# Performance work log

Hardware: AMD Instinct MI355X
Metric: run time of the kernel (lower is better)

The kernel has to match this reference:

```python
import jax, jax.numpy as jnp
import numpy as np

C_IN, C_OUT, ORDER, BATCH, N = 4, 8, 3, 8, 512
STDV = 1.0 / 3.0


def setup_inputs() -> dict:
    key = jax.random.key(0)
    k0, k1, k2, k3, k4 = jax.random.split(key, 5)
    s_in = jax.random.normal(k0, (C_IN, BATCH, N, N), dtype=jnp.float32)
    a_o = jax.random.normal(k1, (BATCH, N, N), dtype=jnp.float32)
    alpha = jax.random.normal(k2, (C_OUT, C_IN), dtype=jnp.float32) * STDV + 1.0
    beta = jax.random.normal(k3, (C_OUT, C_IN), dtype=jnp.float32) * STDV + 0.0
    coeffs = jax.random.normal(k4, (C_OUT, ORDER + 1, C_IN), dtype=jnp.float32) * STDV
    coeffs = coeffs.at[:, 1, :].set(1.0)  # torch init sets linear Cheb coeff to 1
    tau = jnp.linspace(0.01, 0.9, C_OUT).astype(jnp.float32).reshape(C_OUT, 1, 1, 1)
    return {"s_in": s_in, "a_o": a_o, "alpha": alpha, "beta": beta,
            "coeffs": coeffs, "tau": tau}


def _cheb_terms(A, n_terms):
    # Chebyshev matrix polynomial basis: T0=I, T1=A, T_k = 2*A@T_{k-1} - T_{k-2}
    b, n, _ = A.shape
    terms = [jnp.broadcast_to(jnp.eye(n, dtype=A.dtype), (b, n, n)), A]
    for _ in range(2, n_terms):
        terms.append(2.0 * jnp.matmul(A, terms[-1]) - terms[-2])
    return jnp.stack(terms[:n_terms])  # (n_terms, b, n, n)


def reference(s_in, a_o, alpha, beta, coeffs, tau):
    # s_in: (c_in, B, N, N); a_o: (B, N, N)
    c_out, n_terms, c_in = coeffs.shape
    n = a_o.shape[-1]
    # mimo_tensor_polynomial with cob='cheb': a_o is identical across c_in,
    # so compute the Cheb basis once on (B,N,N) and contract with coeffs.
    T = _cheb_terms(a_o, n_terms)                      # (K+1, B, N, N)
    poly = jnp.einsum('oki,kbnm->oibnm', coeffs, T)    # (c_out, c_in, B, N, N)
    # a@a_o + a_o@a is independent of c_out (broadcast in torch), compute once
    mix = jnp.matmul(s_in, a_o) + jnp.matmul(a_o, s_in)  # (c_in, B, N, N)
    temp = (alpha[:, :, None, None, None] * s_in
            + beta[:, :, None, None, None] * mix
            + poly)                                     # (c_out, c_in, B, N, N)
    zd = 1.0 - jnp.eye(n, dtype=temp.dtype)             # zero diagonal mask
    temp = temp * zd
    temp = jnp.mean(temp, axis=1)                       # (c_out, B, N, N)
    # normalize_slices(which_norm='max_abs'): per (c_out, batch) slice
    mx = jnp.max(jnp.abs(temp), axis=(-2, -1), keepdims=True)
    temp = temp / jnp.where(mx == 0, jnp.ones_like(mx), mx)
    return jax.nn.relu(temp - tau)
```

## Files before the change

### kernel.cpp

```cpp
#include <hip/hip_runtime.h>

#define NDIM 512
#define NN (512*512)

typedef float          fv4  __attribute__((ext_vector_type(4)));
typedef unsigned int   uv2  __attribute__((ext_vector_type(2)));
typedef unsigned int   uv4  __attribute__((ext_vector_type(4)));
typedef unsigned short usv4 __attribute__((ext_vector_type(4)));
typedef unsigned short usv8 __attribute__((ext_vector_type(8)));
typedef short          sv8  __attribute__((ext_vector_type(8)));

__device__ __forceinline__ unsigned short f2bf(float x){
    unsigned u = __builtin_bit_cast(unsigned, x);
    u += 0x7fffu + ((u >> 16) & 1u);
    return (unsigned short)(u >> 16);
}
__device__ __forceinline__ float bf2f(unsigned short s){
    unsigned u = ((unsigned)s) << 16;
    return __builtin_bit_cast(float, u);
}

#define MFMA16(acc, va, vb) \
    acc = __builtin_amdgcn_mfma_f32_16x16x32_bf16( \
        __builtin_bit_cast(sv8, va), __builtin_bit_cast(sv8, vb), acc, 0, 0, 0)

#define TRREAD(dst, addr) \
    asm volatile("ds_read_b64_tr_b16 %0, %1" : "=v"(dst) : "v"(addr))

__global__ __launch_bounds__(256) void preconv_kernel(
    const float* __restrict__ s_in, const float* __restrict__ a_o,
    unsigned short* __restrict__ s_bf, unsigned short* __restrict__ Ah,
    unsigned short* __restrict__ Al)
{
    const int z  = blockIdx.y;
    const int e0 = blockIdx.x * 1024 + threadIdx.x * 4;
    if (z < 32) {
        float4 v = *(const float4*)(s_in + z * NN + e0);
        float vv[4] = {v.x, v.y, v.z, v.w};
        usv4 o;
        #pragma unroll
        for (int j = 0; j < 4; ++j) o[j] = f2bf(vv[j]);
        *(usv4*)(s_bf + z * NN + e0) = o;
    } else {
        const int b = z - 32;
        float4 v = *(const float4*)(a_o + b * NN + e0);
        float vv[4] = {v.x, v.y, v.z, v.w};
        usv4 h, l;
        #pragma unroll
        for (int j = 0; j < 4; ++j) {
            unsigned short hb = f2bf(vv[j]);
            h[j] = hb;
            l[j] = f2bf(vv[j] - bf2f(hb));
        }
        *(usv4*)(Ah + b * NN + e0) = h;
        *(usv4*)(Al + b * NN + e0) = l;
    }
}

__device__ __forceinline__ void stage_x8(const unsigned short* __restrict__ X,
                                         int row0, int k0, int tid,
                                         unsigned short (*__restrict__ H)[40]){
    #pragma unroll
    for (int it = 0; it < 2; ++it) {
        int f = tid + it * 256;
        int r = f >> 2, c8 = (f & 3) << 3;
        *(usv8*)&H[r][c8] = *(const usv8*)(X + (row0 + r) * NDIM + k0 + c8);
    }
}
__device__ __forceinline__ void stage_b8(const unsigned short* __restrict__ Y,
                                         int col0, int k0, int tid,
                                         unsigned short* __restrict__ Bs){
    #pragma unroll
    for (int it = 0; it < 2; ++it) {
        int f  = tid + it * 256;
        int kl = f & 3, h = (f >> 2) & 1, cs = (f >> 3) & 7, kh = f >> 6;
        int k  = kh * 4 + kl;
        *(usv8*)&Bs[cs * 512 + k * 16 + h * 8] =
            *(const usv8*)(Y + (k0 + k) * NDIM + col0 + cs * 16 + h * 8);
    }
}

__global__ __launch_bounds__(256) void gemm_fused_kernel(
    const unsigned short* __restrict__ s_bf,
    const unsigned short* __restrict__ Ah, const unsigned short* __restrict__ Al,
    unsigned short* __restrict__ AAh, unsigned short* __restrict__ AAl,
    float* __restrict__ AA, float* __restrict__ AAA,
    unsigned short* __restrict__ MIXbf, int stage)
{
    const int z = blockIdx.z;
    const bool split = (stage == 0) || (z < 8);

    const unsigned short *X1, *X2, *Y1, *Y2;
    if (stage == 0)      { X1 = Ah + z * NN;  X2 = Al + z * NN;
                           Y1 = Ah + z * NN;  Y2 = Al + z * NN; }
    else if (z < 8)      { X1 = Ah + z * NN;  X2 = Al + z * NN;
                           Y1 = AAh + z * NN; Y2 = AAl + z * NN; }
    else                 { const int z2 = z - 8, b = z2 & 7;
                           X1 = s_bf + z2 * NN; X2 = Ah + b * NN;
                           Y1 = Ah + b * NN;    Y2 = s_bf + z2 * NN; }

    const int row0 = blockIdx.y * 128, col0 = blockIdx.x * 128;
    const int tid = threadIdx.x, lane = tid & 63, w = tid >> 6;

    __shared__ unsigned short Xa[128][40], Xb[128][40];
    __shared__ unsigned short Ba[4096], Bb[4096];

    fv4 acc[4][4];
    #pragma unroll
    for (int mi = 0; mi < 4; ++mi)
        #pragma unroll
        for (int ni = 0; ni < 4; ++ni) acc[mi][ni] = (fv4)0.f;

    const unsigned ba_base = (unsigned)(uintptr_t)&Ba[0];
    const unsigned bb_base = (unsigned)(uintptr_t)&Bb[0];
    const unsigned laneoff = (((unsigned)lane >> 4) << 7) | (((unsigned)lane & 15) << 3);
    const unsigned wcol    = ((unsigned)(w & 1)) << 12;

    for (int k0 = 0; k0 < NDIM; k0 += 32) {
        stage_x8(X1, row0, k0, tid, Xa);
        stage_x8(X2, row0, k0, tid, Xb);
        stage_b8(Y1, col0, k0, tid, Ba);
        stage_b8(Y2, col0, k0, tid, Bb);
        __syncthreads();

        uv2 fa[4][2], fb[4][2];
        #pragma unroll
        for (int ni = 0; ni < 4; ++ni)
            #pragma unroll
            for (int h = 0; h < 2; ++h) {
                TRREAD(fa[ni][h], ba_base + wcol + laneoff + ni * 1024 + h * 512);
                TRREAD(fb[ni][h], bb_base + wcol + laneoff + ni * 1024 + h * 512);
            }
        asm volatile("s_waitcnt lgkmcnt(0)" ::: "memory");
        __builtin_amdgcn_sched_barrier(0);

        const int g4 = (lane >> 4) * 4;
        #pragma unroll
        for (int mi = 0; mi < 4; ++mi) {
            const unsigned short* xr1 = &Xa[(w >> 1) * 64 + mi * 16 + (lane & 15)][0];
            const unsigned short* xr2 = &Xb[(w >> 1) * 64 + mi * 16 + (lane & 15)][0];
            uv2 a0 = *(const uv2*)(xr1 + g4);
            uv2 a1 = *(const uv2*)(xr1 + 16 + g4);
            uv2 b0 = *(const uv2*)(xr2 + g4);
            uv2 b1 = *(const uv2*)(xr2 + 16 + g4);
            uv4 xa = {a0.x, a0.y, a1.x, a1.y};
            uv4 xb = {b0.x, b0.y, b1.x, b1.y};
            #pragma unroll
            for (int ni = 0; ni < 4; ++ni) {
                uv4 vba = {fa[ni][0].x, fa[ni][0].y, fa[ni][1].x, fa[ni][1].y};
                uv4 vbb = {fb[ni][0].x, fb[ni][0].y, fb[ni][1].x, fb[ni][1].y};
                if (split) {
                    MFMA16(acc[mi][ni], xa, vba);
                    MFMA16(acc[mi][ni], xa, vbb);
                    MFMA16(acc[mi][ni], xb, vba);
                } else {
                    MFMA16(acc[mi][ni], xa, vba);
                    MFMA16(acc[mi][ni], xb, vbb);
                }
            }
        }
        __syncthreads();
    }

    const int g = lane >> 4, c15 = lane & 15;
    if (split) {
        float* C = (stage == 0) ? (AA + z * NN) : (AAA + z * NN);
        #pragma unroll
        for (int mi = 0; mi < 4; ++mi)
            #pragma unroll
            for (int ni = 0; ni < 4; ++ni) {
                int r = row0 + (w >> 1) * 64 + mi * 16 + g * 4;
                int c = col0 + (w & 1) * 64 + ni * 16 + c15;
                #pragma unroll
                for (int q = 0; q < 4; ++q) {
                    float v = acc[mi][ni][q];
                    C[(r + q) * NDIM + c] = v;
                    if (stage == 0) {
                        unsigned short hb = f2bf(v);
                        AAh[z * NN + (r + q) * NDIM + c] = hb;
                        AAl[z * NN + (r + q) * NDIM + c] = f2bf(v - bf2f(hb));
                    }
                }
            }
    } else {
        unsigned short* Cm = MIXbf + (z - 8) * NN;
        #pragma unroll
        for (int mi = 0; mi < 4; ++mi)
            #pragma unroll
            for (int ni = 0; ni < 4; ++ni) {
                int r = row0 + (w >> 1) * 64 + mi * 16 + g * 4;
                int c = col0 + (w & 1) * 64 + ni * 16 + c15;
                #pragma unroll
                for (int q = 0; q < 4; ++q)
                    Cm[(r + q) * NDIM + c] = f2bf(acc[mi][ni][q]);
            }
    }
}

__global__ __launch_bounds__(256) void combine_kernel(
    const unsigned short* __restrict__ s_bf, const unsigned short* __restrict__ Ah,
    const float* __restrict__ AA, const float* __restrict__ AAA,
    const unsigned short* __restrict__ MIXbf,
    const float* __restrict__ alpha, const float* __restrict__ beta,
    const float* __restrict__ coeffs,
    float* __restrict__ out, unsigned short* __restrict__ tmp,
    unsigned int* __restrict__ smax, int use_tmp)
{
    const int b  = blockIdx.y;
    const int e0 = blockIdx.x * 2048 + threadIdx.x * 8;
    const int n  = e0 >> 9;
    const int m0 = e0 & 511;

    float ca[8], cb[8], cc[8];
    #pragma unroll
    for (int o = 0; o < 8; ++o) {
        float c1 = 0.f, c2 = 0.f, c3 = 0.f;
        #pragma unroll
        for (int i = 0; i < 4; ++i) {
            c1 += coeffs[o * 16 + 4 + i];
            c2 += coeffs[o * 16 + 8 + i];
            c3 += coeffs[o * 16 + 12 + i];
        }
        ca[o] = c1 - 3.f * c3; cb[o] = 2.f * c2; cc[o] = 4.f * c3;
    }

    float av[8], aav[8], aaav[8], sv[4][8], mv[4][8];
    {
        usv8 a8 = *(const usv8*)(Ah + b * NN + e0);
        #pragma unroll
        for (int j = 0; j < 8; ++j) av[j] = bf2f(a8[j]);
        const float4 q0 = *(const float4*)(AA + b * NN + e0);
        const float4 q1 = *(const float4*)(AA + b * NN + e0 + 4);
        aav[0]=q0.x; aav[1]=q0.y; aav[2]=q0.z; aav[3]=q0.w;
        aav[4]=q1.x; aav[5]=q1.y; aav[6]=q1.z; aav[7]=q1.w;
        const float4 r0 = *(const float4*)(AAA + b * NN + e0);
        const float4 r1 = *(const float4*)(AAA + b * NN + e0 + 4);
        aaav[0]=r0.x; aaav[1]=r0.y; aaav[2]=r0.z; aaav[3]=r0.w;
        aaav[4]=r1.x; aaav[5]=r1.y; aaav[6]=r1.z; aaav[7]=r1.w;
        #pragma unroll
        for (int i = 0; i < 4; ++i) {
            usv8 s8 = *(const usv8*)(s_bf + (i * 8 + b) * NN + e0);
            usv8 m8 = *(const usv8*)(MIXbf + (i * 8 + b) * NN + e0);
            #pragma unroll
            for (int j = 0; j < 8; ++j) { sv[i][j] = bf2f(s8[j]); mv[i][j] = bf2f(m8[j]); }
        }
    }

    float lmax[8];
    #pragma unroll
    for (int o = 0; o < 8; ++o) {
        float outv[8];
        float lm = 0.f;
        #pragma unroll
        for (int j = 0; j < 8; ++j) {
            float t = ca[o] * av[j] + cb[o] * aav[j] + cc[o] * aaav[j];
            #pragma unroll
            for (int i = 0; i < 4; ++i)
                t += alpha[o * 4 + i] * sv[i][j] + beta[o * 4 + i] * mv[i][j];
            t *= 0.25f;
            if (n == m0 + j) t = 0.f;
            outv[j] = t;
            lm = fmaxf(lm, fabsf(t));
        }
        lmax[o] = lm;
        if (use_tmp) {
            usv8 ov;
            #pragma unroll
            for (int j = 0; j < 8; ++j) ov[j] = f2bf(outv[j]);
            *(usv8*)(tmp + (o * 8 + b) * NN + e0) = ov;
        } else {
            *(float4*)(out + (o * 8 + b) * NN + e0) =
                make_float4(outv[0], outv[1], outv[2], outv[3]);
            *(float4*)(out + (o * 8 + b) * NN + e0 + 4) =
                make_float4(outv[4], outv[5], outv[6], outv[7]);
        }
    }

    #pragma unroll
    for (int o = 0; o < 8; ++o) {
        #pragma unroll
        for (int off = 32; off > 0; off >>= 1)
            lmax[o] = fmaxf(lmax[o], __shfl_xor(lmax[o], off, 64));
    }
    __shared__ float red[4][8];
    const int lane = threadIdx.x & 63, wv = threadIdx.x >> 6;
    if (lane == 0) {
        #pragma unroll
        for (int o = 0; o < 8; ++o) red[wv][o] = lmax[o];
    }
    __syncthreads();
    if (threadIdx.x < 8) {
        const int o = threadIdx.x;
        const float mfin = fmaxf(fmaxf(red[0][o], red[1][o]), fmaxf(red[2][o], red[3][o]));
        atomicMax(&smax[o * 8 + b], __float_as_uint(mfin));
    }
}

__global__ __launch_bounds__(256) void norm_kernel(
    float* __restrict__ out, const unsigned short* __restrict__ tmp,
    const unsigned int* __restrict__ smax, const float* __restrict__ tau,
    int use_tmp)
{
    const int ob = blockIdx.y;
    const float mx = __uint_as_float(smax[ob]);
    const float inv = (mx == 0.f) ? 1.f : (1.f / mx);
    const float t = tau[ob >> 3];
    const int e0 = blockIdx.x * 2048 + threadIdx.x * 8;
    float v[8];
    if (use_tmp) {
        usv8 tv = *(const usv8*)(tmp + ob * NN + e0);
        #pragma unroll
        for (int j = 0; j < 8; ++j) v[j] = bf2f(tv[j]);
    } else {
        float4 v0 = *(float4*)(out + ob * NN + e0);
        float4 v1 = *(float4*)(out + ob * NN + e0 + 4);
        v[0]=v0.x; v[1]=v0.y; v[2]=v0.z; v[3]=v0.w;
        v[4]=v1.x; v[5]=v1.y; v[6]=v1.z; v[7]=v1.w;
    }
    #pragma unroll
    for (int j = 0; j < 8; ++j) v[j] = fmaxf(fmaf(v[j], inv, -t), 0.f);
    *(float4*)(out + ob * NN + e0)     = make_float4(v[0], v[1], v[2], v[3]);
    *(float4*)(out + ob * NN + e0 + 4) = make_float4(v[4], v[5], v[6], v[7]);
}

extern "C" void kernel_launch(void* const* d_in, const int* in_sizes, int n_in,
                              void* d_out, int out_size, void* d_ws, size_t ws_size,
                              hipStream_t stream) {
    (void)in_sizes; (void)n_in; (void)out_size;
    const float* s_in   = (const float*)d_in[0];
    const float* a_o    = (const float*)d_in[1];
    const float* alpha  = (const float*)d_in[2];
    const float* beta   = (const float*)d_in[3];
    const float* coeffs = (const float*)d_in[4];
    const float* tau    = (const float*)d_in[5];
    float* out = (float*)d_out;

    float* AA  = (float*)d_ws;
    float* AAA = AA + 8 * NN;
    unsigned short* s_bf  = (unsigned short*)(AAA + 8 * NN);
    unsigned short* Ah    = s_bf + 32 * NN;
    unsigned short* Al    = Ah + 8 * NN;
    unsigned short* AAh   = Al + 8 * NN;
    unsigned short* AAl   = AAh + 8 * NN;
    unsigned short* MIXbf = AAl + 8 * NN;
    unsigned int* SMAX = (unsigned int*)(MIXbf + 32 * NN);
    unsigned short* TMP = (unsigned short*)(SMAX + 64);

    const size_t need_tmp = (size_t)((char*)(TMP + 64 * NN) - (char*)d_ws);
    const int use_tmp = (ws_size >= need_tmp) ? 1 : 0;

    hipLaunchKernelGGL(preconv_kernel, dim3(256, 40), dim3(256), 0, stream,
                       s_in, a_o, s_bf, Ah, Al);
    hipLaunchKernelGGL(gemm_fused_kernel, dim3(4, 4, 8), dim3(256), 0, stream,
                       s_bf, Ah, Al, AAh, AAl, AA, AAA, MIXbf, 0);
    hipLaunchKernelGGL(gemm_fused_kernel, dim3(4, 4, 40), dim3(256), 0, stream,
                       s_bf, Ah, Al, AAh, AAl, AA, AAA, MIXbf, 1);
    hipMemsetAsync(SMAX, 0, 64 * sizeof(unsigned int), stream);
    hipLaunchKernelGGL(combine_kernel, dim3(128, 8), dim3(256), 0, stream,
                       s_bf, Ah, AA, AAA, MIXbf, alpha, beta, coeffs,
                       out, TMP, SMAX, use_tmp);
    hipLaunchKernelGGL(norm_kernel, dim3(128, 64), dim3(256), 0, stream,
                       out, TMP, SMAX, tau, use_tmp);
}
```

Measured before the change: 253.9 us.

## Double-buffer LDS tiles and prefetch next K-slice into registers

Turns the GEMM main loop into a two-stage software pipeline. The next K-slice's global loads go into registers before the current tile's MFMA work, and are written to the alternate LDS buffer afterwards, so only one barrier per iteration remains. The aim is to hide global memory latency behind compute. In exchange it doubles LDS use per block and adds eight live usv8 registers per thread, which may lower occupancy.

```diff
diff --git a/kernel.cpp b/kernel.cpp
--- a/kernel.cpp
+++ b/kernel.cpp
@@ -57,29 +57,6 @@
     }
 }
 
-__device__ __forceinline__ void stage_x8(const unsigned short* __restrict__ X,
-                                         int row0, int k0, int tid,
-                                         unsigned short (*__restrict__ H)[40]){
-    #pragma unroll
-    for (int it = 0; it < 2; ++it) {
-        int f = tid + it * 256;
-        int r = f >> 2, c8 = (f & 3) << 3;
-        *(usv8*)&H[r][c8] = *(const usv8*)(X + (row0 + r) * NDIM + k0 + c8);
-    }
-}
-__device__ __forceinline__ void stage_b8(const unsigned short* __restrict__ Y,
-                                         int col0, int k0, int tid,
-                                         unsigned short* __restrict__ Bs){
-    #pragma unroll
-    for (int it = 0; it < 2; ++it) {
-        int f  = tid + it * 256;
-        int kl = f & 3, h = (f >> 2) & 1, cs = (f >> 3) & 7, kh = f >> 6;
-        int k  = kh * 4 + kl;
-        *(usv8*)&Bs[cs * 512 + k * 16 + h * 8] =
-            *(const usv8*)(Y + (k0 + k) * NDIM + col0 + cs * 16 + h * 8);
-    }
-}
-
 __global__ __launch_bounds__(256) void gemm_fused_kernel(
     const unsigned short* __restrict__ s_bf,
     const unsigned short* __restrict__ Ah, const unsigned short* __restrict__ Al,
@@ -102,8 +79,8 @@
     const int row0 = blockIdx.y * 128, col0 = blockIdx.x * 128;
     const int tid = threadIdx.x, lane = tid & 63, w = tid >> 6;
 
-    __shared__ unsigned short Xa[128][40], Xb[128][40];
-    __shared__ unsigned short Ba[4096], Bb[4096];
+    __shared__ unsigned short Xa[2][128][40], Xb[2][128][40];
+    __shared__ unsigned short Ba[2][4096], Bb[2][4096];
 
     fv4 acc[4][4];
     #pragma unroll
@@ -111,18 +88,45 @@
         #pragma unroll
         for (int ni = 0; ni < 4; ++ni) acc[mi][ni] = (fv4)0.f;
 
-    const unsigned ba_base = (unsigned)(uintptr_t)&Ba[0];
-    const unsigned bb_base = (unsigned)(uintptr_t)&Bb[0];
+    const int xr  = tid >> 2, xc = (tid & 3) << 3;
+    const int xo0 = (row0 + xr) * NDIM + xc;
+    const int xo1 = xo0 + 64 * NDIM;
+    const int kl = tid & 3, hh = (tid >> 2) & 1, cs = (tid >> 3) & 7, kh = tid >> 6;
+    const int kb0 = kh * 4 + kl;
+    const int yo0 = kb0 * NDIM + col0 + cs * 16 + hh * 8;
+    const int yo1 = yo0 + 16 * NDIM;
+    const int lb0 = cs * 512 + kb0 * 16 + hh * 8;
+    const int lb1 = lb0 + 256;
+
     const unsigned laneoff = (((unsigned)lane >> 4) << 7) | (((unsigned)lane & 15) << 3);
     const unsigned wcol    = ((unsigned)(w & 1)) << 12;
-
-    for (int k0 = 0; k0 < NDIM; k0 += 32) {
-        stage_x8(X1, row0, k0, tid, Xa);
-        stage_x8(X2, row0, k0, tid, Xb);
-        stage_b8(Y1, col0, k0, tid, Ba);
-        stage_b8(Y2, col0, k0, tid, Bb);
-        __syncthreads();
-
+    const int g4 = (lane >> 4) * 4;
+
+    usv8 lx1a, lx1b, lx2a, lx2b, ly1a, ly1b, ly2a, ly2b;
+
+    auto gload = [&](int k0) {
+        lx1a = *(const usv8*)(X1 + xo0 + k0);
+        lx1b = *(const usv8*)(X1 + xo1 + k0);
+        lx2a = *(const usv8*)(X2 + xo0 + k0);
+        lx2b = *(const usv8*)(X2 + xo1 + k0);
+        ly1a = *(const usv8*)(Y1 + yo0 + k0 * NDIM);
+        ly1b = *(const usv8*)(Y1 + yo1 + k0 * NDIM);
+        ly2a = *(const usv8*)(Y2 + yo0 + k0 * NDIM);
+        ly2b = *(const usv8*)(Y2 + yo1 + k0 * NDIM);
+    };
+    auto swrite = [&](int buf) {
+        *(usv8*)&Xa[buf][xr][xc]      = lx1a;
+        *(usv8*)&Xa[buf][64 + xr][xc] = lx1b;
+        *(usv8*)&Xb[buf][xr][xc]      = lx2a;
+        *(usv8*)&Xb[buf][64 + xr][xc] = lx2b;
+        *(usv8*)&Ba[buf][lb0] = ly1a;
+        *(usv8*)&Ba[buf][lb1] = ly1b;
+        *(usv8*)&Bb[buf][lb0] = ly2a;
+        *(usv8*)&Bb[buf][lb1] = ly2b;
+    };
+    auto compute = [&](int buf) {
+        const unsigned ba_base = (unsigned)(uintptr_t)&Ba[buf][0];
+        const unsigned bb_base = (unsigned)(uintptr_t)&Bb[buf][0];
         uv2 fa[4][2], fb[4][2];
         #pragma unroll
         for (int ni = 0; ni < 4; ++ni)
@@ -134,33 +138,44 @@
         asm volatile("s_waitcnt lgkmcnt(0)" ::: "memory");
         __builtin_amdgcn_sched_barrier(0);
 
-        const int g4 = (lane >> 4) * 4;
         #pragma unroll
         for (int mi = 0; mi < 4; ++mi) {
-            const unsigned short* xr1 = &Xa[(w >> 1) * 64 + mi * 16 + (lane & 15)][0];
-            const unsigned short* xr2 = &Xb[(w >> 1) * 64 + mi * 16 + (lane & 15)][0];
+            const unsigned short* xr1 = &Xa[buf][(w >> 1) * 64 + mi * 16 + (lane & 15)][0];
+            const unsigned short* xr2 = &Xb[buf][(w >> 1) * 64 + mi * 16 + (lane & 15)][0];
             uv2 a0 = *(const uv2*)(xr1 + g4);
             uv2 a1 = *(const uv2*)(xr1 + 16 + g4);
             uv2 b0 = *(const uv2*)(xr2 + g4);
             uv2 b1 = *(const uv2*)(xr2 + 16 + g4);
-            uv4 xa = {a0.x, a0.y, a1.x, a1.y};
-            uv4 xb = {b0.x, b0.y, b1.x, b1.y};
+            uv4 xva = {a0.x, a0.y, a1.x, a1.y};
+            uv4 xvb = {b0.x, b0.y, b1.x, b1.y};
             #pragma unroll
             for (int ni = 0; ni < 4; ++ni) {
                 uv4 vba = {fa[ni][0].x, fa[ni][0].y, fa[ni][1].x, fa[ni][1].y};
                 uv4 vbb = {fb[ni][0].x, fb[ni][0].y, fb[ni][1].x, fb[ni][1].y};
                 if (split) {
-                    MFMA16(acc[mi][ni], xa, vba);
-                    MFMA16(acc[mi][ni], xa, vbb);
-                    MFMA16(acc[mi][ni], xb, vba);
+                    MFMA16(acc[mi][ni], xva, vba);
+                    MFMA16(acc[mi][ni], xva, vbb);
+                    MFMA16(acc[mi][ni], xvb, vba);
                 } else {
-                    MFMA16(acc[mi][ni], xa, vba);
-                    MFMA16(acc[mi][ni], xb, vbb);
+                    MFMA16(acc[mi][ni], xva, vba);
+                    MFMA16(acc[mi][ni], xvb, vbb);
                 }
             }
         }
+    };
+
+    gload(0);
+    swrite(0);
+    __syncthreads();
+    int cur = 0;
+    for (int t = 0; t < 15; ++t) {
+        gload((t + 1) * 32);
+        compute(cur);
+        swrite(cur ^ 1);
         __syncthreads();
-    }
+        cur ^= 1;
+    }
+    compute(cur);
 
     const int g = lane >> 4, c15 = lane & 15;
     if (split) {
```

Result: faster. 225.9 us (-11.0%).
